# Kernel tuning notes

Hardware: AMD Instinct MI355X
Metric: run time of the kernel (lower is better)

The kernel has to match this reference:

```python
import jax, jax.numpy as jnp
import numpy as np

N = 100000      # nodes
E = 1600000     # edges (avg degree 16)
G = 1000        # graphs in batch
F_IN = 128      # num_features
C = 10          # num_classes
EPS = 1e-5


def setup_inputs() -> dict:
    key = jax.random.key(0)
    ks = jax.random.split(key, 12)
    w = lambda k, shape: jax.random.normal(k, shape, jnp.float32) * 0.05
    return {
        'x': jax.random.normal(ks[0], (N, F_IN), jnp.float32),
        'edge_index': jax.random.randint(ks[1], (2, E), 0, N, jnp.int32),
        'edge_weights': jax.random.randint(ks[2], (E,), 0, 2, jnp.int32),
        'batch': jnp.sort(jax.random.randint(ks[3], (N,), 0, G, jnp.int32)),
        'num_graphs': G,
        # initial MLP: Linear(128,32)+BN+ReLU, Linear(32,32)+BN+ReLU
        'W1': w(ks[4], (F_IN, 32)), 'b1': jnp.zeros(32), 'g1': jnp.ones(32), 'bt1': jnp.zeros(32),
        'W2': w(ks[5], (32, 32)), 'b2': jnp.zeros(32), 'g2': jnp.ones(32), 'bt2': jnp.zeros(32),
        'Wl0': w(ks[6], (32, C)), 'bl0': jnp.zeros(C),   # initial_linear
        'Wg1': w(ks[7], (32, 64)), 'bg1': jnp.zeros(64),  # GCNConv 1
        'Wl1': w(ks[8], (64, C)), 'bl1': jnp.zeros(C),
        'Wg2': w(ks[9], (64, 64)), 'bg2': jnp.zeros(64),  # GCNConv 2
        'Wl2': w(ks[10], (64, C)), 'bl2': jnp.zeros(C),
    }


def _bn(h, gamma, beta):
    # BatchNorm1d in training mode: biased batch statistics over nodes
    mu = h.mean(0)
    var = ((h - mu) ** 2).mean(0)
    return gamma * (h - mu) * jax.lax.rsqrt(var + EPS) + beta


def _gcn(h_in, row, col, w, W, b):
    # PyG GCNConv with self-loops: D^{-1/2}(A+I)D^{-1/2} X W + b,
    # edges with mask weight 0 contribute nothing (incl. to degree).
    n = h_in.shape[0]
    h = h_in @ W
    deg = jax.ops.segment_sum(w, col, num_segments=n) + 1.0  # +1 self-loop
    dinv = jax.lax.rsqrt(deg)
    norm = w * dinv[row] * dinv[col]                  # [E]
    agg = jax.ops.segment_sum(h[row] * norm[:, None], col, num_segments=n)
    agg = agg + h * (dinv * dinv)[:, None]            # self-loop term
    return agg + b


def _pool_max(h, batch, num_graphs):
    # torch_scatter scatter_max readout; empty segments -> 0
    p = jax.ops.segment_max(h, batch, num_segments=num_graphs)
    return jnp.where(jnp.isfinite(p), p, 0.0)


def reference(x, edge_index, edge_weights, batch, num_graphs,
              W1, b1, g1, bt1, W2, b2, g2, bt2, Wl0, bl0,
              Wg1, bg1, Wl1, bl1, Wg2, bg2, Wl2, bl2):
    row, col = edge_index[0], edge_index[1]
    w = (edge_weights == 1).astype(x.dtype)  # boolean edge mask as 0/1 weight
    # initial MLP (dropout treated as identity for deterministic reference)
    h = jax.nn.relu(_bn(x @ W1 + b1, g1, bt1))
    h = jax.nn.relu(_bn(h @ W2 + b2, g2, bt2))
    out = _pool_max(h @ Wl0 + bl0, batch, num_graphs)
    # layer 1
    h = _gcn(h, row, col, w, Wg1, bg1)
    out = out + _pool_max(h, batch, num_graphs) @ Wl1 + bl1
    # layer 2
    h = _gcn(h, row, col, w, Wg2, bg2)
    out = out + _pool_max(h, batch, num_graphs) @ Wl2 + bl2
    return out
```

## Files before the change

kernel.cpp:

```cpp
#include <hip/hip_runtime.h>

#define NN 100000
#define EE 1600000
#define GG 1000
#define BN_EPS 1e-5f
#define NB1 391

__device__ __forceinline__ unsigned encf(float f){
  unsigned u = __float_as_uint(f);
  return (u & 0x80000000u) ? ~u : (u | 0x80000000u);
}
__device__ __forceinline__ float dec0(unsigned e){
  unsigned u = (e & 0x80000000u) ? (e & 0x7fffffffu) : ~e;
  float f = __uint_as_float(u);
  return isfinite(f) ? f : 0.0f;
}
__device__ __forceinline__ unsigned short f2bf(float f){
  unsigned u = __float_as_uint(f);
  u += 0x7FFFu + ((u >> 16) & 1u);
  return (unsigned short)(u >> 16);
}
__device__ __forceinline__ float bf2f(unsigned short s){
  return __uint_as_float(((unsigned)s) << 16);
}

__global__ void k_count(const int* __restrict__ ei, const int* __restrict__ ew,
                        int* __restrict__ cnt){
  int e = blockIdx.x*256 + threadIdx.x;
  if (e < EE && ew[e] == 1) atomicAdd(&cnt[ei[EE + e]], 1);
}

__global__ __launch_bounds__(256) void k_scan1(const int* __restrict__ cnt,
    int* __restrict__ loc, int* __restrict__ bsum){
  __shared__ int sm[256];
  const int i = blockIdx.x*256 + threadIdx.x;
  const int v = (i < NN) ? cnt[i] : 0;
  sm[threadIdx.x] = v;
  __syncthreads();
  for (int off = 1; off < 256; off <<= 1){
    int t = (threadIdx.x >= off) ? sm[threadIdx.x - off] : 0;
    __syncthreads();
    sm[threadIdx.x] += t;
    __syncthreads();
  }
  if (i < NN) loc[i] = sm[threadIdx.x] - v;
  if (threadIdx.x == 255) bsum[blockIdx.x] = sm[255];
}

__global__ __launch_bounds__(512) void k_scan2(const int* __restrict__ bsum,
    int* __restrict__ boff){
  __shared__ int sm[512];
  const int t = threadIdx.x;
  const int v = (t < NB1) ? bsum[t] : 0;
  sm[t] = v;
  __syncthreads();
  for (int off = 1; off < 512; off <<= 1){
    int x = (t >= off) ? sm[t - off] : 0;
    __syncthreads();
    sm[t] += x;
    __syncthreads();
  }
  if (t <= NB1) boff[t] = sm[t] - v;
}

__global__ void k_fin(const int* __restrict__ cnt, const int* __restrict__ loc,
                      const int* __restrict__ boff, float* __restrict__ dinv,
                      int* __restrict__ rowstart, int* __restrict__ fill){
  const int i = blockIdx.x*256 + threadIdx.x;
  if (i < NN){
    int rs = loc[i] + boff[i >> 8];
    rowstart[i] = rs; fill[i] = rs;
    dinv[i] = rsqrtf((float)cnt[i] + 1.0f);
  } else if (i == NN){
    rowstart[NN] = boff[NB1];
  }
}

__global__ void k_scatter(const int* __restrict__ ei, const int* __restrict__ ew,
                          int* __restrict__ fill, int* __restrict__ csr){
  int e = blockIdx.x*256 + threadIdx.x;
  if (e < EE && ew[e] == 1){
    int c = ei[EE + e];
    int pos = atomicAdd(&fill[c], 1);
    csr[pos] = ei[e];
  }
}

__global__ __launch_bounds__(256) void k_gemm1(const float* __restrict__ x,
    const float* __restrict__ W1, const float* __restrict__ b1,
    float* __restrict__ Y1, float* __restrict__ stats){
  __shared__ float xs[32*132];
  __shared__ float Ws[128*32];
  __shared__ float red[64];
  const int tid = threadIdx.x;
  for (int j = tid; j < 1024; j += 256) ((float4*)Ws)[j] = ((const float4*)W1)[j];
  const int r = tid >> 3, cg = tid & 7;
  const float4 bv = ((const float4*)b1)[cg];
  float s0=0,s1=0,s2=0,s3=0,q0=0,q1=0,q2=0,q3=0;
  for (int tile = blockIdx.x; tile < 3125; tile += gridDim.x){
    __syncthreads();
    for (int j = tid; j < 1024; j += 256){
      int rr = j >> 5, kk = j & 31;
      *(float4*)&xs[rr*132 + kk*4] = ((const float4*)x)[(size_t)tile*1024 + j];
    }
    __syncthreads();
    float a0=bv.x, a1=bv.y, a2=bv.z, a3=bv.w;
    const float* xr = &xs[r*132];
    const float* wc = &Ws[cg*4];
    #pragma unroll 8
    for (int k = 0; k < 128; k++){
      float xv = xr[k];
      float4 w = *(const float4*)&wc[k*32];
      a0 += xv*w.x; a1 += xv*w.y; a2 += xv*w.z; a3 += xv*w.w;
    }
    float4 o; o.x=a0; o.y=a1; o.z=a2; o.w=a3;
    ((float4*)Y1)[(size_t)(tile*32 + r)*8 + cg] = o;
    s0+=a0; s1+=a1; s2+=a2; s3+=a3;
    q0+=a0*a0; q1+=a1*a1; q2+=a2*a2; q3+=a3*a3;
  }
  __syncthreads();
  if (tid < 64) red[tid] = 0.f;
  __syncthreads();
  atomicAdd(&red[cg*4+0], s0); atomicAdd(&red[cg*4+1], s1);
  atomicAdd(&red[cg*4+2], s2); atomicAdd(&red[cg*4+3], s3);
  atomicAdd(&red[32+cg*4+0], q0); atomicAdd(&red[32+cg*4+1], q1);
  atomicAdd(&red[32+cg*4+2], q2); atomicAdd(&red[32+cg*4+3], q3);
  __syncthreads();
  if (tid < 64) atomicAdd(&stats[tid], red[tid]);
}

__global__ __launch_bounds__(256) void k_mlp2(const float* __restrict__ Y1,
    const float* __restrict__ W2, const float* __restrict__ b2,
    const float* __restrict__ g1, const float* __restrict__ bt1,
    float* __restrict__ stats, float* __restrict__ Y2){
  __shared__ float hs[32*36];
  __shared__ float Ws[32*32];
  __shared__ float red[64];
  __shared__ float scs[32], shs[32];
  const int tid = threadIdx.x;
  ((float4*)Ws)[tid] = ((const float4*)W2)[tid];
  if (tid < 32){
    float mean = stats[tid] * (1.0f/NN);
    float var  = stats[32 + tid] * (1.0f/NN) - mean*mean;
    float s = g1[tid] * rsqrtf(fmaxf(var, 0.0f) + BN_EPS);
    scs[tid] = s; shs[tid] = bt1[tid] - mean*s;
  }
  __syncthreads();
  const int r = tid >> 3, cg = tid & 7;
  const float4 bv = ((const float4*)b2)[cg];
  const float4 sc = *(const float4*)&scs[cg*4];
  const float4 sh = *(const float4*)&shs[cg*4];
  float s0=0,s1=0,s2=0,s3=0,q0=0,q1=0,q2=0,q3=0;
  for (int tile = blockIdx.x; tile < 3125; tile += gridDim.x){
    __syncthreads();
    {
      float4 v = ((const float4*)Y1)[(size_t)tile*256 + tid];
      v.x = fmaxf(fmaf(v.x, sc.x, sh.x), 0.f);
      v.y = fmaxf(fmaf(v.y, sc.y, sh.y), 0.f);
      v.z = fmaxf(fmaf(v.z, sc.z, sh.z), 0.f);
      v.w = fmaxf(fmaf(v.w, sc.w, sh.w), 0.f);
      *(float4*)&hs[r*36 + cg*4] = v;
    }
    __syncthreads();
    float a0=bv.x, a1=bv.y, a2=bv.z, a3=bv.w;
    const float* hr = &hs[r*36];
    const float* wc = &Ws[cg*4];
    #pragma unroll
    for (int k = 0; k < 32; k++){
      float h = hr[k];
      float4 w = *(const float4*)&wc[k*32];
      a0 += h*w.x; a1 += h*w.y; a2 += h*w.z; a3 += h*w.w;
    }
    float4 o; o.x=a0; o.y=a1; o.z=a2; o.w=a3;
    ((float4*)Y2)[(size_t)(tile*32 + r)*8 + cg] = o;
    s0+=a0; s1+=a1; s2+=a2; s3+=a3;
    q0+=a0*a0; q1+=a1*a1; q2+=a2*a2; q3+=a3*a3;
  }
  __syncthreads();
  if (tid < 64) red[tid] = 0.f;
  __syncthreads();
  atomicAdd(&red[cg*4+0], s0); atomicAdd(&red[cg*4+1], s1);
  atomicAdd(&red[cg*4+2], s2); atomicAdd(&red[cg*4+3], s3);
  atomicAdd(&red[32+cg*4+0], q0); atomicAdd(&red[32+cg*4+1], q1);
  atomicAdd(&red[32+cg*4+2], q2); atomicAdd(&red[32+cg*4+3], q3);
  __syncthreads();
  if (tid < 64) atomicAdd(&stats[128 + tid], red[tid]);
}

__global__ __launch_bounds__(256) void k_layer0(const float* __restrict__ Y2,
    const float* __restrict__ stats, const float* __restrict__ g2,
    const float* __restrict__ bt2, const float* __restrict__ Wg1,
    const float* __restrict__ Wl0, const float* __restrict__ bl0,
    const float* __restrict__ dinv, const int* __restrict__ batch,
    unsigned short* __restrict__ Hs1, unsigned* __restrict__ Pool0){
  __shared__ float hs[32*36];
  __shared__ float Wg[32*64];
  __shared__ float Wl[320];
  __shared__ float bl[10];
  __shared__ float scs[32], shs[32];
  const int tid = threadIdx.x;
  ((float4*)Wg)[tid]       = ((const float4*)Wg1)[tid];
  ((float4*)Wg)[tid + 256] = ((const float4*)Wg1)[tid + 256];
  for (int j = tid; j < 320; j += 256) Wl[j] = Wl0[j];
  if (tid < 10)  bl[tid] = bl0[tid];
  if (tid < 32){
    float mean = stats[128 + tid] * (1.0f/NN);
    float var  = stats[160 + tid] * (1.0f/NN) - mean*mean;
    float s = g2[tid] * rsqrtf(fmaxf(var, 0.0f) + BN_EPS);
    scs[tid] = s; shs[tid] = bt2[tid] - mean*s;
  }
  __syncthreads();
  {
    const int rr = tid >> 3, kk = tid & 7;
    const float4 sc = *(const float4*)&scs[kk*4];
    const float4 sh = *(const float4*)&shs[kk*4];
    float4 v = ((const float4*)Y2)[(size_t)blockIdx.x*256 + tid];
    v.x = fmaxf(fmaf(v.x, sc.x, sh.x), 0.f);
    v.y = fmaxf(fmaf(v.y, sc.y, sh.y), 0.f);
    v.z = fmaxf(fmaf(v.z, sc.z, sh.z), 0.f);
    v.w = fmaxf(fmaf(v.w, sc.w, sh.w), 0.f);
    *(float4*)&hs[rr*36 + kk*4] = v;
  }
  __syncthreads();
  const int w = tid >> 6, f = tid & 63;
  for (int i = 0; i < 8; i++){
    const int r = w*8 + i;
    const int row = blockIdx.x*32 + r;
    const float* hr = &hs[r*36];
    float acc = 0.f;
    #pragma unroll
    for (int k = 0; k < 32; k++) acc += hr[k]*Wg[k*64 + f];
    Hs1[(size_t)row*64 + f] = f2bf(acc * dinv[row]);
    if (f < 10){
      float p = bl[f];
      #pragma unroll
      for (int k = 0; k < 32; k++) p += hr[k]*Wl[k*10 + f];
      atomicMax(&Pool0[batch[row]*10 + f], encf(p));
    }
  }
}

template<bool GEMM>
__global__ __launch_bounds__(256) void k_agg(const unsigned short* __restrict__ Hs,
    const float* __restrict__ dinv, const int* __restrict__ rowstart,
    const int* __restrict__ csr, const float* __restrict__ bias,
    const int* __restrict__ batch, const float* __restrict__ Wg2,
    unsigned short* __restrict__ Hs2out, unsigned* __restrict__ Pool){
  __shared__ float sm[4][64];
  __shared__ int sb[4];
  __shared__ float WgL[GEMM ? 64*64 : 4];
  const int tid = threadIdx.x;
  if (GEMM){
    #pragma unroll
    for (int j = 0; j < 4; j++)
      ((float4*)WgL)[tid + j*256] = ((const float4*)Wg2)[tid + j*256];
  }
  const int w = tid >> 6, f = tid & 63;
  const int c = blockIdx.x*4 + w;
  const int s = rowstart[c], e = rowstart[c+1];
  float acc = 0.f;
  int j = s;
  for (; j + 3 < e; j += 4){
    const int r0 = csr[j], r1 = csr[j+1], r2 = csr[j+2], r3 = csr[j+3];
    acc += bf2f(Hs[(size_t)r0*64 + f]);
    acc += bf2f(Hs[(size_t)r1*64 + f]);
    acc += bf2f(Hs[(size_t)r2*64 + f]);
    acc += bf2f(Hs[(size_t)r3*64 + f]);
  }
  for (; j < e; j++) acc += bf2f(Hs[(size_t)csr[j]*64 + f]);
  const float dc = dinv[c];
  const float h = fmaf(acc + bf2f(Hs[(size_t)c*64 + f]), dc, bias[f]);
  sm[w][f] = h;
  if (f == 0) sb[w] = batch[c];
  __syncthreads();
  if (w == 0){
    const int b0 = sb[0], b1 = sb[1], b2 = sb[2], b3 = sb[3];
    if (b0 == b3){
      float m = fmaxf(fmaxf(sm[0][f], sm[1][f]), fmaxf(sm[2][f], sm[3][f]));
      atomicMax(&Pool[b0*64 + f], encf(m));
    } else {
      atomicMax(&Pool[b0*64 + f], encf(sm[0][f]));
      atomicMax(&Pool[b1*64 + f], encf(sm[1][f]));
      atomicMax(&Pool[b2*64 + f], encf(sm[2][f]));
      atomicMax(&Pool[b3*64 + f], encf(sm[3][f]));
    }
  }
  if (GEMM){
    float ga = 0.f;
    const float* hr = sm[w];
    #pragma unroll 16
    for (int k = 0; k < 64; k++) ga = fmaf(hr[k], WgL[k*64 + f], ga);
    Hs2out[(size_t)c*64 + f] = f2bf(ga * dc);
  }
}

__global__ __launch_bounds__(256) void k_final(const unsigned* __restrict__ P0,
    const unsigned* __restrict__ P1, const unsigned* __restrict__ P2,
    const float* __restrict__ Wl1, const float* __restrict__ bl1,
    const float* __restrict__ Wl2, const float* __restrict__ bl2,
    float* __restrict__ out){
  const int t = blockIdx.x*256 + threadIdx.x;
  const int g = t >> 4, c = t & 15;
  if (g >= GG || c >= 10) return;
  float acc = dec0(P0[g*10 + c]) + bl1[c] + bl2[c];
  for (int f = 0; f < 64; f++){
    acc += dec0(P1[g*64 + f]) * Wl1[f*10 + c];
    acc += dec0(P2[g*64 + f]) * Wl2[f*10 + c];
  }
  out[g*10 + c] = acc;
}

extern "C" void kernel_launch(void* const* d_in, const int* in_sizes, int n_in,
                              void* d_out, int out_size, void* d_ws, size_t ws_size,
                              hipStream_t stream){
  const float* x   = (const float*)d_in[0];
  const int*   ei  = (const int*)d_in[1];
  const int*   ew  = (const int*)d_in[2];
  const int*   bat = (const int*)d_in[3];
  const float* W1  = (const float*)d_in[5],  *b1  = (const float*)d_in[6];
  const float* g1  = (const float*)d_in[7],  *bt1 = (const float*)d_in[8];
  const float* W2  = (const float*)d_in[9],  *b2  = (const float*)d_in[10];
  const float* g2  = (const float*)d_in[11], *bt2 = (const float*)d_in[12];
  const float* Wl0 = (const float*)d_in[13], *bl0 = (const float*)d_in[14];
  const float* Wg1 = (const float*)d_in[15], *bg1 = (const float*)d_in[16];
  const float* Wl1 = (const float*)d_in[17], *bl1 = (const float*)d_in[18];
  const float* Wg2 = (const float*)d_in[19], *bg2 = (const float*)d_in[20];
  const float* Wl2 = (const float*)d_in[21], *bl2 = (const float*)d_in[22];

  float* ws = (float*)d_ws;
  const size_t oCnt   = 0;
  const size_t oStats = NN;
  const size_t oP0    = oStats + 256;
  const size_t oP1    = oP0 + (size_t)GG*10;
  const size_t oP2    = oP1 + (size_t)GG*64;
  const size_t oZEnd  = oP2 + (size_t)GG*64;
  const size_t oDinv  = oZEnd;
  const size_t oLoc   = oDinv + NN;
  const size_t oBsum  = oLoc + NN;
  const size_t oBoff  = oBsum + 512;
  const size_t oRS    = oBoff + 512;
  const size_t oFill  = oRS + NN + 8;
  const size_t oCsr   = oFill + NN;
  const size_t oA     = oCsr + EE;
  const size_t oHs1   = oA + (size_t)NN*64;

  int*   cnt   = (int*)(ws + oCnt);
  float* stats = ws + oStats;
  unsigned* P0 = (unsigned*)(ws + oP0);
  unsigned* P1 = (unsigned*)(ws + oP1);
  unsigned* P2 = (unsigned*)(ws + oP2);
  float* dinv  = ws + oDinv;
  int*   loc   = (int*)(ws + oLoc);
  int*   bsum  = (int*)(ws + oBsum);
  int*   boff  = (int*)(ws + oBoff);
  int*   rs    = (int*)(ws + oRS);
  int*   fill  = (int*)(ws + oFill);
  int*   csr   = (int*)(ws + oCsr);
  float* Y1    = ws + oA;
  float* Y2    = ws + oA + (size_t)NN*32;
  unsigned short* Hs2 = (unsigned short*)(ws + oA);
  unsigned short* Hs1 = (unsigned short*)(ws + oHs1);

  (void)hipMemsetAsync(d_ws, 0, oZEnd*sizeof(float), stream);

  k_count  <<<EE/256, 256, 0, stream>>>(ei, ew, cnt);
  k_scan1  <<<NB1, 256, 0, stream>>>(cnt, loc, bsum);
  k_scan2  <<<1, 512, 0, stream>>>(bsum, boff);
  k_fin    <<<NB1, 256, 0, stream>>>(cnt, loc, boff, dinv, rs, fill);
  k_scatter<<<EE/256, 256, 0, stream>>>(ei, ew, fill, csr);

  k_gemm1<<<1536, 256, 0, stream>>>(x, W1, b1, Y1, stats);
  k_mlp2 <<<1536, 256, 0, stream>>>(Y1, W2, b2, g1, bt1, stats, Y2);
  k_layer0<<<3125, 256, 0, stream>>>(Y2, stats, g2, bt2, Wg1, Wl0, bl0, dinv, bat, Hs1, P0);
  k_agg<true> <<<NN/4, 256, 0, stream>>>(Hs1, dinv, rs, csr, bg1, bat, Wg2, Hs2, P1);
  k_agg<false><<<NN/4, 256, 0, stream>>>(Hs2, dinv, rs, csr, bg2, bat, nullptr, nullptr, P2);
  k_final<<<(GG*16 + 255)/256, 256, 0, stream>>>(P0, P1, P2, Wl1, bl1, Wl2, bl2, (float*)d_out);
}
```

Baseline: 338.4 us.

## Split layer-2 GEMM out of aggregation kernel and widen gather unroll

The 64x64 GEMM that was fused into the first aggregation kernel moves into its own tiled kernel. That kernel reads the bf16 layer-1 output back in 32-row blocks and keeps the weights in shared memory. The first aggregation kernel no longer loads a 16KB weight tile per 4-node block, which should cut its LDS footprint and raise occupancy for the latency-bound gather. The cost is an extra kernel launch plus a write and read of a 100000x64 bf16 intermediate. The gather loop is also unrolled to 8 neighbours with a tree-style sum to allow more loads in flight.

```diff
diff --git a/kernel.cpp b/kernel.cpp
--- a/kernel.cpp
+++ b/kernel.cpp
@@ -240,36 +240,38 @@
   }
 }
 
-template<bool GEMM>
-__global__ __launch_bounds__(256) void k_agg(const unsigned short* __restrict__ Hs,
-    const float* __restrict__ dinv, const int* __restrict__ rowstart,
-    const int* __restrict__ csr, const float* __restrict__ bias,
-    const int* __restrict__ batch, const float* __restrict__ Wg2,
-    unsigned short* __restrict__ Hs2out, unsigned* __restrict__ Pool){
-  __shared__ float sm[4][64];
-  __shared__ int sb[4];
-  __shared__ float WgL[GEMM ? 64*64 : 4];
-  const int tid = threadIdx.x;
-  if (GEMM){
-    #pragma unroll
-    for (int j = 0; j < 4; j++)
-      ((float4*)WgL)[tid + j*256] = ((const float4*)Wg2)[tid + j*256];
-  }
-  const int w = tid >> 6, f = tid & 63;
-  const int c = blockIdx.x*4 + w;
-  const int s = rowstart[c], e = rowstart[c+1];
+__device__ __forceinline__ float gather_sum(const unsigned short* __restrict__ Hs,
+    const int* __restrict__ csr, int s, int e, int f){
   float acc = 0.f;
   int j = s;
+  for (; j + 7 < e; j += 8){
+    const int r0 = csr[j],   r1 = csr[j+1], r2 = csr[j+2], r3 = csr[j+3];
+    const int r4 = csr[j+4], r5 = csr[j+5], r6 = csr[j+6], r7 = csr[j+7];
+    float t0 = bf2f(Hs[(size_t)r0*64 + f]);
+    float t1 = bf2f(Hs[(size_t)r1*64 + f]);
+    float t2 = bf2f(Hs[(size_t)r2*64 + f]);
+    float t3 = bf2f(Hs[(size_t)r3*64 + f]);
+    float t4 = bf2f(Hs[(size_t)r4*64 + f]);
+    float t5 = bf2f(Hs[(size_t)r5*64 + f]);
+    float t6 = bf2f(Hs[(size_t)r6*64 + f]);
+    float t7 = bf2f(Hs[(size_t)r7*64 + f]);
+    acc += ((t0 + t1) + (t2 + t3)) + ((t4 + t5) + (t6 + t7));
+  }
   for (; j + 3 < e; j += 4){
     const int r0 = csr[j], r1 = csr[j+1], r2 = csr[j+2], r3 = csr[j+3];
-    acc += bf2f(Hs[(size_t)r0*64 + f]);
-    acc += bf2f(Hs[(size_t)r1*64 + f]);
-    acc += bf2f(Hs[(size_t)r2*64 + f]);
-    acc += bf2f(Hs[(size_t)r3*64 + f]);
+    float t0 = bf2f(Hs[(size_t)r0*64 + f]);
+    float t1 = bf2f(Hs[(size_t)r1*64 + f]);
+    float t2 = bf2f(Hs[(size_t)r2*64 + f]);
+    float t3 = bf2f(Hs[(size_t)r3*64 + f]);
+    acc += (t0 + t1) + (t2 + t3);
   }
   for (; j < e; j++) acc += bf2f(Hs[(size_t)csr[j]*64 + f]);
-  const float dc = dinv[c];
-  const float h = fmaf(acc + bf2f(Hs[(size_t)c*64 + f]), dc, bias[f]);
+  return acc;
+}
+
+__device__ __forceinline__ void pool_epilogue(float h, int w, int f, int c,
+    const int* __restrict__ batch, unsigned* __restrict__ Pool,
+    float (*sm)[64], int* sb){
   sm[w][f] = h;
   if (f == 0) sb[w] = batch[c];
   __syncthreads();
@@ -285,12 +287,66 @@
       atomicMax(&Pool[b3*64 + f], encf(sm[3][f]));
     }
   }
-  if (GEMM){
-    float ga = 0.f;
-    const float* hr = sm[w];
-    #pragma unroll 16
-    for (int k = 0; k < 64; k++) ga = fmaf(hr[k], WgL[k*64 + f], ga);
-    Hs2out[(size_t)c*64 + f] = f2bf(ga * dc);
+}
+
+__global__ __launch_bounds__(256) void k_agg1(const unsigned short* __restrict__ Hs,
+    const float* __restrict__ dinv, const int* __restrict__ rowstart,
+    const int* __restrict__ csr, const float* __restrict__ bias,
+    const int* __restrict__ batch, unsigned short* __restrict__ H2b,
+    unsigned* __restrict__ Pool){
+  __shared__ float sm[4][64];
+  __shared__ int sb[4];
+  const int w = threadIdx.x >> 6, f = threadIdx.x & 63;
+  const int c = blockIdx.x*4 + w;
+  const int s = rowstart[c], e = rowstart[c+1];
+  float acc = gather_sum(Hs, csr, s, e, f);
+  const float dc = dinv[c];
+  const float h = fmaf(acc + bf2f(Hs[(size_t)c*64 + f]), dc, bias[f]);
+  H2b[(size_t)c*64 + f] = f2bf(h);
+  pool_epilogue(h, w, f, c, batch, Pool, sm, sb);
+}
+
+__global__ __launch_bounds__(256) void k_agg2(const unsigned short* __restrict__ Hs,
+    const float* __restrict__ dinv, const int* __restrict__ rowstart,
+    const int* __restrict__ csr, const float* __restrict__ bias,
+    const int* __restrict__ batch, unsigned* __restrict__ Pool){
+  __shared__ float sm[4][64];
+  __shared__ int sb[4];
+  const int w = threadIdx.x >> 6, f = threadIdx.x & 63;
+  const int c = blockIdx.x*4 + w;
+  const int s = rowstart[c], e = rowstart[c+1];
+  float acc = gather_sum(Hs, csr, s, e, f);
+  const float dc = dinv[c];
+  const float h = fmaf(acc + bf2f(Hs[(size_t)c*64 + f]), dc, bias[f]);
+  pool_epilogue(h, w, f, c, batch, Pool, sm, sb);
+}
+
+__global__ __launch_bounds__(256) void k_layer1(const unsigned short* __restrict__ H2b,
+    const float* __restrict__ Wg2, const float* __restrict__ dinv,
+    unsigned short* __restrict__ Hs2){
+  __shared__ float as[32*68];
+  __shared__ float Wg[64*64];
+  const int tid = threadIdx.x;
+  #pragma unroll
+  for (int j = 0; j < 4; j++) ((float4*)Wg)[tid + j*256] = ((const float4*)Wg2)[tid + j*256];
+  {
+    const int rr = tid >> 3, kk = tid & 7;
+    ushort4 v0 = ((const ushort4*)H2b)[(size_t)blockIdx.x*512 + tid*2];
+    ushort4 v1 = ((const ushort4*)H2b)[(size_t)blockIdx.x*512 + tid*2 + 1];
+    float* dst = &as[rr*68 + kk*8];
+    dst[0]=bf2f(v0.x); dst[1]=bf2f(v0.y); dst[2]=bf2f(v0.z); dst[3]=bf2f(v0.w);
+    dst[4]=bf2f(v1.x); dst[5]=bf2f(v1.y); dst[6]=bf2f(v1.z); dst[7]=bf2f(v1.w);
+  }
+  __syncthreads();
+  const int w = tid >> 6, f = tid & 63;
+  for (int i = 0; i < 8; i++){
+    const int r = w*8 + i;
+    const int row = blockIdx.x*32 + r;
+    const float* ar = &as[r*68];
+    float acc = 0.f;
+    #pragma unroll
+    for (int k = 0; k < 64; k++) acc += ar[k]*Wg[k*64 + f];
+    Hs2[(size_t)row*64 + f] = f2bf(acc * dinv[row]);
   }
 }
 
@@ -358,8 +414,9 @@
   int*   csr   = (int*)(ws + oCsr);
   float* Y1    = ws + oA;
   float* Y2    = ws + oA + (size_t)NN*32;
-  unsigned short* Hs2 = (unsigned short*)(ws + oA);
+  unsigned short* H2b = (unsigned short*)(ws + oA);
   unsigned short* Hs1 = (unsigned short*)(ws + oHs1);
+  unsigned short* Hs2 = (unsigned short*)(ws + oA + (size_t)NN*32);
 
   (void)hipMemsetAsync(d_ws, 0, oZEnd*sizeof(float), stream);
 
@@ -372,7 +429,8 @@
   k_gemm1<<<1536, 256, 0, stream>>>(x, W1, b1, Y1, stats);
   k_mlp2 <<<1536, 256, 0, stream>>>(Y1, W2, b2, g1, bt1, stats, Y2);
   k_layer0<<<3125, 256, 0, stream>>>(Y2, stats, g2, bt2, Wg1, Wl0, bl0, dinv, bat, Hs1, P0);
-  k_agg<true> <<<NN/4, 256, 0, stream>>>(Hs1, dinv, rs, csr, bg1, bat, Wg2, Hs2, P1);
-  k_agg<false><<<NN/4, 256, 0, stream>>>(Hs2, dinv, rs, csr, bg2, bat, nullptr, nullptr, P2);
+  k_agg1 <<<NN/4, 256, 0, stream>>>(Hs1, dinv, rs, csr, bg1, bat, H2b, P1);
+  k_layer1<<<3125, 256, 0, stream>>>(H2b, Wg2, dinv, Hs2);
+  k_agg2 <<<NN/4, 256, 0, stream>>>(Hs2, dinv, rs, csr, bg2, bat, P2);
   k_final<<<(GG*16 + 255)/256, 256, 0, stream>>>(P0, P1, P2, Wl1, bl1, Wl2, bl2, (float*)d_out);
 }
```

After: 336.8 us. No clear change (-0.5%).
